# Optimization experiments

Measured on AMD Instinct MI355X. Metric: run time of the kernel, lower is better.

The kernel has to match this reference:

```python
import jax, jax.numpy as jnp
import numpy as np

N = 50000      # number of atoms/nodes
D = 32         # atom_dim == units (pad_length = 0)
E = 300000     # number of bonds/edges
BD = 16        # bond_dim
STEPS = 4      # message passing steps


def setup_inputs() -> dict:
    key = jax.random.key(0)
    ks = jax.random.split(key, 8)
    atom_features = jax.random.normal(ks[0], (N, D), dtype=jnp.float32)
    bond_features = jax.random.uniform(ks[1], (E, BD), dtype=jnp.float32)
    pair_indices = jax.random.randint(ks[2], (E, 2), 0, N, dtype=jnp.int32)
    # EdgeNetwork kernel: xavier_uniform on [bond_dim, atom_dim*atom_dim]
    s = float(np.sqrt(6.0 / (BD + D * D)))
    kernel = jax.random.uniform(ks[3], (BD, D * D), dtype=jnp.float32, minval=-s, maxval=s)
    bias = jnp.zeros((D * D,), dtype=jnp.float32)
    # torch.nn.GRUCell init: U(-1/sqrt(H), 1/sqrt(H)), H = D (pad_length = 0)
    stdv = float(1.0 / np.sqrt(D))
    W_ih = jax.random.uniform(ks[4], (3 * D, D), dtype=jnp.float32, minval=-stdv, maxval=stdv)
    W_hh = jax.random.uniform(ks[5], (3 * D, D), dtype=jnp.float32, minval=-stdv, maxval=stdv)
    b_ih = jax.random.uniform(ks[6], (3 * D,), dtype=jnp.float32, minval=-stdv, maxval=stdv)
    b_hh = jax.random.uniform(ks[7], (3 * D,), dtype=jnp.float32, minval=-stdv, maxval=stdv)
    return {
        "atom_features": atom_features,
        "bond_features": bond_features,
        "pair_indices": pair_indices,
        "kernel": kernel,
        "bias": bias,
        "W_ih": W_ih,
        "W_hh": W_hh,
        "b_ih": b_ih,
        "b_hh": b_hh,
    }


def _gru_cell(x, h, W_ih, W_hh, b_ih, b_hh):
    # torch.nn.GRUCell math, gates stacked as (r, z, n)
    gi = x @ W_ih.T + b_ih  # [N, 3D]
    gh = h @ W_hh.T + b_hh  # [N, 3D]
    i_r, i_z, i_n = jnp.split(gi, 3, axis=-1)
    h_r, h_z, h_n = jnp.split(gh, 3, axis=-1)
    r = jax.nn.sigmoid(i_r + h_r)
    z = jax.nn.sigmoid(i_z + h_z)
    n = jnp.tanh(i_n + r * h_n)
    return (1.0 - z) * n + z * h


def reference(atom_features, bond_features, pair_indices, kernel, bias, W_ih, W_hh, b_ih, b_hh):
    # pad_length = units - atom_dim = 0, so no padding needed.
    W = kernel.reshape(BD, D, D)   # per-bond-feature DxD transforms
    Bm = bias.reshape(D, D)        # bias as DxD matrix applied to neighbor feats
    dst = pair_indices[:, 0]       # aggregation (index_add) target
    src = pair_indices[:, 1]       # gathered neighbor

    h = atom_features
    for _ in range(STEPS):
        nbr = h[src]  # [E, D] gather
        # transformed[e, i] = sum_j (bond[e] @ kernel + bias)[i, j] * nbr[e, j]
        msg = jnp.einsum('eb,bij,ej->ei', bond_features, W, nbr) + nbr @ Bm.T
        agg = jax.ops.segment_sum(msg, dst, num_segments=N)  # scatter-add
        h = _gru_cell(agg, h, W_ih, W_hh, b_ih, b_hh)
    return h
```

## Files before the change

kernel.cpp:

```cpp
#include <hip/hip_runtime.h>
#include <math.h>

#define N_ATOMS 50000
#define D 32
#define E_EDGES 300000
#define BD 16
#define SW 544
#define SCAN_BLOCKS ((N_ATOMS + 255) / 256)
#define GRU_TILE 8
#define GRU_NT (N_ATOMS / GRU_TILE)

#define NB 32
#define FBLOCKS ((N_ATOMS + NB - 1) / NB)

__device__ __forceinline__ float sigmoidf_(float x) {
    return 1.0f / (1.0f + __expf(-x));
}


__global__ void k_build_wt(const float* __restrict__ kern,
                           const float* __restrict__ bias,
                           float* __restrict__ WTj) {
    int idx = blockIdx.x * 256 + threadIdx.x;
    if (idx >= 32 * SW) return;
    int j = idx / SW;
    int r = idx - j * SW;
    int b = r >> 5, i = r & 31;
    WTj[idx] = (b < BD) ? kern[b * 1024 + i * 32 + j] : bias[i * 32 + j];
}

__global__ void k_hist(const int* __restrict__ pair, int* __restrict__ deg) {
    int e = blockIdx.x * 256 + threadIdx.x;
    if (e < E_EDGES) atomicAdd(&deg[pair[2 * e + 1]], 1);
}

__global__ void k_scan1(const int* __restrict__ deg, int* __restrict__ offs,
                        int* __restrict__ bsums) {
    __shared__ int sm[256];
    int t = threadIdx.x, gid = blockIdx.x * 256 + t;
    int v = (gid < N_ATOMS) ? deg[gid] : 0;
    sm[t] = v;
    __syncthreads();
    for (int off = 1; off < 256; off <<= 1) {
        int x = (t >= off) ? sm[t - off] : 0;
        __syncthreads();
        sm[t] += x;
        __syncthreads();
    }
    if (gid < N_ATOMS) offs[gid] = sm[t] - v;
    if (t == 255) bsums[blockIdx.x] = sm[255];
}

__global__ void k_scan2(const int* __restrict__ bsums, int* __restrict__ boffs, int nb) {
    __shared__ int sm[256];
    int t = threadIdx.x;
    int v = (t < nb) ? bsums[t] : 0;
    sm[t] = v;
    __syncthreads();
    for (int off = 1; off < 256; off <<= 1) {
        int x = (t >= off) ? sm[t - off] : 0;
        __syncthreads();
        sm[t] += x;
        __syncthreads();
    }
    if (t < nb) boffs[t] = sm[t] - v;
}

__global__ void k_scan3(int* __restrict__ offs, const int* __restrict__ boffs) {
    int gid = blockIdx.x * 256 + threadIdx.x;
    if (gid < N_ATOMS) offs[gid] += boffs[blockIdx.x];
}

__global__ void k_scatter_perm(const int* __restrict__ pair, const int* __restrict__ offs,
                               int* __restrict__ cursor, const float* __restrict__ bond,
                               float* __restrict__ bond_perm, int* __restrict__ dst_perm) {
    int e = blockIdx.x * 256 + threadIdx.x;
    if (e >= E_EDGES) return;
    int d = pair[2 * e], s = pair[2 * e + 1];
    int pos = offs[s] + atomicAdd(&cursor[s], 1);
    dst_perm[pos] = d;
    const float4* src4 = (const float4*)(bond + (size_t)e * BD);
    float4* dst4 = (float4*)(bond_perm + (size_t)pos * BD);
    dst4[0] = src4[0];
    dst4[1] = src4[1];
    dst4[2] = src4[2];
    dst4[3] = src4[3];
}

#define EDGE_FMA(M, B0, B1, B2, B3, YN) do {            \
    M = fmaf(B0.x, YN[0],  M); M = fmaf(B0.y, YN[1],  M); \
    M = fmaf(B0.z, YN[2],  M); M = fmaf(B0.w, YN[3],  M); \
    M = fmaf(B1.x, YN[4],  M); M = fmaf(B1.y, YN[5],  M); \
    M = fmaf(B1.z, YN[6],  M); M = fmaf(B1.w, YN[7],  M); \
    M = fmaf(B2.x, YN[8],  M); M = fmaf(B2.y, YN[9],  M); \
    M = fmaf(B2.z, YN[10], M); M = fmaf(B2.w, YN[11], M); \
    M = fmaf(B3.x, YN[12], M); M = fmaf(B3.y, YN[13], M); \
    M = fmaf(B3.z, YN[14], M); M = fmaf(B3.w, YN[15], M); \
} while (0)

__global__ __launch_bounds__(256, 2)
void k_fused(const float* __restrict__ h_in, float* __restrict__ agg,
             const float* __restrict__ bond_perm, const int* __restrict__ dst_perm,
             const float* __restrict__ WTj,
             const int* __restrict__ offs, const int* __restrict__ deg) {
    __shared__ float h_lds[NB][33];

    const int t = threadIdx.x;
    const int bbase = blockIdx.x * NB;
    const int i = t & 31;
    const int grp = t >> 5;
    const int hn0 = grp * 4;

#pragma unroll
    for (int k = 0; k < 4; ++k) {
        const int idx = t + 256 * k;
        const int n = idx >> 5, j = idx & 31;
        const int node = bbase + n;
        h_lds[n][j] = (node < N_ATOMS) ? h_in[(size_t)node * D + j] : 0.f;
    }

    int stv[4], env[4];
#pragma unroll
    for (int n = 0; n < 4; ++n) {
        const int node = bbase + hn0 + n;
        const bool ok = (node < N_ATOMS);
        const int o = ok ? offs[node] : 0;
        stv[n] = o;
        env[n] = o + (ok ? deg[node] : 0);
    }
    __syncthreads();

    float y[4][17];
#pragma unroll
    for (int n = 0; n < 4; ++n)
#pragma unroll
        for (int b = 0; b < 17; ++b) y[n][b] = 0.f;

    for (int j = 0; j < 32; ++j) {
        float wv[17];
#pragma unroll
        for (int b = 0; b < 17; ++b)
            wv[b] = WTj[j * SW + b * 32 + i];
#pragma unroll
        for (int n = 0; n < 4; ++n) {
            const float hv = h_lds[hn0 + n][j];
#pragma unroll
            for (int b = 0; b < 17; ++b)
                y[n][b] = fmaf(wv[b], hv, y[n][b]);
        }
    }

#pragma unroll
    for (int n = 0; n < 4; ++n) {
        int p = stv[n];
        const int e = env[n];
        for (; p + 2 <= e; p += 2) {
            const float4* bp0 = (const float4*)(bond_perm + (size_t)p * BD);
            const float4* bp1 = (const float4*)(bond_perm + (size_t)(p + 1) * BD);
            const int d0 = dst_perm[p];
            const int d1 = dst_perm[p + 1];
            const float4 a0 = bp0[0], a1 = bp0[1], a2 = bp0[2], a3 = bp0[3];
            const float4 c0 = bp1[0], c1 = bp1[1], c2 = bp1[2], c3 = bp1[3];
            float m0 = y[n][16];
            float m1 = y[n][16];
            EDGE_FMA(m0, a0, a1, a2, a3, y[n]);
            EDGE_FMA(m1, c0, c1, c2, c3, y[n]);
            atomicAdd(&agg[(size_t)d0 * D + i], m0);
            atomicAdd(&agg[(size_t)d1 * D + i], m1);
        }
        if (p < e) {
            const float4* bp0 = (const float4*)(bond_perm + (size_t)p * BD);
            const int d0 = dst_perm[p];
            const float4 a0 = bp0[0], a1 = bp0[1], a2 = bp0[2], a3 = bp0[3];
            float m0 = y[n][16];
            EDGE_FMA(m0, a0, a1, a2, a3, y[n]);
            atomicAdd(&agg[(size_t)d0 * D + i], m0);
        }
    }
}

__global__ __launch_bounds__(256, 2)
void k_gru(float* __restrict__ agg_g, const float* __restrict__ h_in,
           float* __restrict__ h_out,
           const float* __restrict__ Wih, const float* __restrict__ Whh,
           const float* __restrict__ bih, const float* __restrict__ bhh) {
    __shared__ float Wih_s[96][33];
    __shared__ float Whh_s[96][33];
    __shared__ float bih_s[96], bhh_s[96];
    __shared__ float x_lds[GRU_TILE][32];
    __shared__ float h_lds[GRU_TILE][32];

    const int t = threadIdx.x;

    for (int idx = t; idx < 96 * 32; idx += 256) {
        const int o = idx >> 5, jj = idx & 31;
        Wih_s[o][jj] = Wih[idx];
        Whh_s[o][jj] = Whh[idx];
    }
    if (t < 96) { bih_s[t] = bih[t]; bhh_s[t] = bhh[t]; }

    const int r = t >> 5;
    const int i = t & 31;
    const int stride = gridDim.x;

    int tile = blockIdx.x;
    float xr = 0.f, hr = 0.f;
    if (tile < GRU_NT) {
        xr = agg_g[tile * 256 + t];
        hr = h_in[tile * 256 + t];
    }
    for (; tile < GRU_NT; tile += stride) {
        ((float*)x_lds)[t] = xr;
        ((float*)h_lds)[t] = hr;
        agg_g[tile * 256 + t] = 0.f;
        __syncthreads();
        const int nxt = tile + stride;
        if (nxt < GRU_NT) {
            xr = agg_g[nxt * 256 + t];
            hr = h_in[nxt * 256 + t];
        }
        float gri = bih_s[i],      grh = bhh_s[i];
        float gzi = bih_s[32 + i], gzh = bhh_s[32 + i];
        float gni = bih_s[64 + i], gnh = bhh_s[64 + i];
#pragma unroll 8
        for (int jj = 0; jj < 32; ++jj) {
            const float xv = x_lds[r][jj];
            const float hv = h_lds[r][jj];
            gri = fmaf(Wih_s[i][jj],      xv, gri);
            gzi = fmaf(Wih_s[32 + i][jj], xv, gzi);
            gni = fmaf(Wih_s[64 + i][jj], xv, gni);
            grh = fmaf(Whh_s[i][jj],      hv, grh);
            gzh = fmaf(Whh_s[32 + i][jj], hv, gzh);
            gnh = fmaf(Whh_s[64 + i][jj], hv, gnh);
        }
        const float rg = sigmoidf_(gri + grh);
        const float zg = sigmoidf_(gzi + gzh);
        float xn = gni + rg * gnh;
        xn = fminf(fmaxf(xn, -15.f), 15.f);
        const float e2 = __expf(2.f * xn);
        const float ng = (e2 - 1.f) / (e2 + 1.f);
        h_out[tile * 256 + t] = (1.f - zg) * ng + zg * h_lds[r][i];
        __syncthreads();
    }
}

extern "C" void kernel_launch(void* const* d_in, const int* in_sizes, int n_in,
                              void* d_out, int out_size, void* d_ws, size_t ws_size,
                              hipStream_t stream) {
    const float* atom = (const float*)d_in[0];
    const float* bond = (const float*)d_in[1];
    const int*   pair = (const int*)d_in[2];
    const float* kern = (const float*)d_in[3];
    const float* bias = (const float*)d_in[4];
    const float* Wih  = (const float*)d_in[5];
    const float* Whh  = (const float*)d_in[6];
    const float* bih  = (const float*)d_in[7];
    const float* bhh  = (const float*)d_in[8];
    float* out = (float*)d_out;

    char* w = (char*)d_ws;
    auto alloc = [&](size_t bytes) {
        char* p = w;
        w += (bytes + 255) & ~size_t(255);
        return p;
    };
    float* hA        = (float*)alloc((size_t)N_ATOMS * D * 4);
    float* aggG      = (float*)alloc((size_t)N_ATOMS * D * 4);
    float* WTj       = (float*)alloc((size_t)32 * SW * 4);
    int*   deg       = (int*)alloc((size_t)N_ATOMS * 4);
    int*   offs      = (int*)alloc((size_t)N_ATOMS * 4);
    int*   cursor    = (int*)alloc((size_t)N_ATOMS * 4);
    int*   bsums     = (int*)alloc(256 * 4);
    int*   boffs     = (int*)alloc(256 * 4);
    int*   dst_perm  = (int*)alloc((size_t)E_EDGES * 4);
    float* bond_perm = (float*)alloc((size_t)E_EDGES * BD * 4);

    hipMemsetAsync(deg, 0, (size_t)N_ATOMS * 4, stream);
    hipMemsetAsync(cursor, 0, (size_t)N_ATOMS * 4, stream);
    hipMemsetAsync(aggG, 0, (size_t)N_ATOMS * D * 4, stream);

    k_build_wt<<<(32 * SW + 255) / 256, 256, 0, stream>>>(kern, bias, WTj);
    k_hist<<<(E_EDGES + 255) / 256, 256, 0, stream>>>(pair, deg);
    k_scan1<<<SCAN_BLOCKS, 256, 0, stream>>>(deg, offs, bsums);
    k_scan2<<<1, 256, 0, stream>>>(bsums, boffs, SCAN_BLOCKS);
    k_scan3<<<SCAN_BLOCKS, 256, 0, stream>>>(offs, boffs);
    k_scatter_perm<<<(E_EDGES + 255) / 256, 256, 0, stream>>>(pair, offs, cursor,
                                                              bond, bond_perm, dst_perm);

    const float* hsrc = atom;
    float* hdst[4] = { hA, out, hA, out };
    for (int s = 0; s < 4; ++s) {
        k_fused<<<FBLOCKS, 256, 0, stream>>>(hsrc, aggG, bond_perm, dst_perm,
                                             WTj, offs, deg);
        k_gru<<<2048, 256, 0, stream>>>(aggG, hsrc, hdst[s], Wih, Whh, bih, bhh);
        hsrc = hdst[s];
    }
}
```

Before: 496.8 us.

## Replace atomic scatter-add with dst-sorted message buffer and segmented reduction

Builds a second CSR grouped by destination node and computes, for each source-sorted edge, its slot in destination order. The message kernel then writes each edge message to that slot with a plain store instead of an atomicAdd. The GRU kernel reduces each node's contiguous message range before the gate math, which also removes the aggregate-buffer memset and the zeroing pass. In exchange it adds a 38 MB message buffer that is written and read every step, plus extra setup kernels for the second histogram, scan and position pass.

```diff
diff --git a/kernel.cpp b/kernel.cpp
--- a/kernel.cpp
+++ b/kernel.cpp
@@ -29,9 +29,9 @@
     WTj[idx] = (b < BD) ? kern[b * 1024 + i * 32 + j] : bias[i * 32 + j];
 }
 
-__global__ void k_hist(const int* __restrict__ pair, int* __restrict__ deg) {
+__global__ void k_hist(const int* __restrict__ pair, int* __restrict__ deg, int col) {
     int e = blockIdx.x * 256 + threadIdx.x;
-    if (e < E_EDGES) atomicAdd(&deg[pair[2 * e + 1]], 1);
+    if (e < E_EDGES) atomicAdd(&deg[pair[2 * e + col]], 1);
 }
 
 __global__ void k_scan1(const int* __restrict__ deg, int* __restrict__ offs,
@@ -73,18 +73,26 @@
 
 __global__ void k_scatter_perm(const int* __restrict__ pair, const int* __restrict__ offs,
                                int* __restrict__ cursor, const float* __restrict__ bond,
-                               float* __restrict__ bond_perm, int* __restrict__ dst_perm) {
+                               float* __restrict__ bond_perm, int* __restrict__ dstid) {
     int e = blockIdx.x * 256 + threadIdx.x;
     if (e >= E_EDGES) return;
     int d = pair[2 * e], s = pair[2 * e + 1];
     int pos = offs[s] + atomicAdd(&cursor[s], 1);
-    dst_perm[pos] = d;
+    dstid[pos] = d;
     const float4* src4 = (const float4*)(bond + (size_t)e * BD);
     float4* dst4 = (float4*)(bond_perm + (size_t)pos * BD);
     dst4[0] = src4[0];
     dst4[1] = src4[1];
     dst4[2] = src4[2];
     dst4[3] = src4[3];
+}
+
+__global__ void k_dstpos(const int* __restrict__ dstid, const int* __restrict__ offs2,
+                         int* __restrict__ cursor2, int* __restrict__ wpos) {
+    int p = blockIdx.x * 256 + threadIdx.x;
+    if (p >= E_EDGES) return;
+    int d = dstid[p];
+    wpos[p] = offs2[d] + atomicAdd(&cursor2[d], 1);
 }
 
 #define EDGE_FMA(M, B0, B1, B2, B3, YN) do {            \
@@ -99,10 +107,10 @@
 } while (0)
 
 __global__ __launch_bounds__(256, 2)
-void k_fused(const float* __restrict__ h_in, float* __restrict__ agg,
-             const float* __restrict__ bond_perm, const int* __restrict__ dst_perm,
-             const float* __restrict__ WTj,
-             const int* __restrict__ offs, const int* __restrict__ deg) {
+void k_msg(const float* __restrict__ h_in, float* __restrict__ msg_d,
+           const float* __restrict__ bond_perm, const int* __restrict__ wpos,
+           const float* __restrict__ WTj,
+           const int* __restrict__ offs, const int* __restrict__ deg) {
     __shared__ float h_lds[NB][33];
 
     const int t = threadIdx.x;
@@ -157,33 +165,34 @@
         for (; p + 2 <= e; p += 2) {
             const float4* bp0 = (const float4*)(bond_perm + (size_t)p * BD);
             const float4* bp1 = (const float4*)(bond_perm + (size_t)(p + 1) * BD);
-            const int d0 = dst_perm[p];
-            const int d1 = dst_perm[p + 1];
+            const int w0 = wpos[p];
+            const int w1 = wpos[p + 1];
             const float4 a0 = bp0[0], a1 = bp0[1], a2 = bp0[2], a3 = bp0[3];
             const float4 c0 = bp1[0], c1 = bp1[1], c2 = bp1[2], c3 = bp1[3];
             float m0 = y[n][16];
             float m1 = y[n][16];
             EDGE_FMA(m0, a0, a1, a2, a3, y[n]);
             EDGE_FMA(m1, c0, c1, c2, c3, y[n]);
-            atomicAdd(&agg[(size_t)d0 * D + i], m0);
-            atomicAdd(&agg[(size_t)d1 * D + i], m1);
+            msg_d[(size_t)w0 * D + i] = m0;
+            msg_d[(size_t)w1 * D + i] = m1;
         }
         if (p < e) {
             const float4* bp0 = (const float4*)(bond_perm + (size_t)p * BD);
-            const int d0 = dst_perm[p];
+            const int w0 = wpos[p];
             const float4 a0 = bp0[0], a1 = bp0[1], a2 = bp0[2], a3 = bp0[3];
             float m0 = y[n][16];
             EDGE_FMA(m0, a0, a1, a2, a3, y[n]);
-            atomicAdd(&agg[(size_t)d0 * D + i], m0);
+            msg_d[(size_t)w0 * D + i] = m0;
         }
     }
 }
 
 __global__ __launch_bounds__(256, 2)
-void k_gru(float* __restrict__ agg_g, const float* __restrict__ h_in,
-           float* __restrict__ h_out,
-           const float* __restrict__ Wih, const float* __restrict__ Whh,
-           const float* __restrict__ bih, const float* __restrict__ bhh) {
+void k_aggru(const float* __restrict__ msg_d,
+             const int* __restrict__ offs2, const int* __restrict__ deg2,
+             const float* __restrict__ h_in, float* __restrict__ h_out,
+             const float* __restrict__ Wih, const float* __restrict__ Whh,
+             const float* __restrict__ bih, const float* __restrict__ bhh) {
     __shared__ float Wih_s[96][33];
     __shared__ float Whh_s[96][33];
     __shared__ float bih_s[96], bhh_s[96];
@@ -203,22 +212,24 @@
     const int i = t & 31;
     const int stride = gridDim.x;
 
-    int tile = blockIdx.x;
-    float xr = 0.f, hr = 0.f;
-    if (tile < GRU_NT) {
-        xr = agg_g[tile * 256 + t];
-        hr = h_in[tile * 256 + t];
-    }
-    for (; tile < GRU_NT; tile += stride) {
-        ((float*)x_lds)[t] = xr;
-        ((float*)h_lds)[t] = hr;
-        agg_g[tile * 256 + t] = 0.f;
-        __syncthreads();
-        const int nxt = tile + stride;
-        if (nxt < GRU_NT) {
-            xr = agg_g[nxt * 256 + t];
-            hr = h_in[nxt * 256 + t];
-        }
+    for (int tile = blockIdx.x; tile < GRU_NT; tile += stride) {
+        const int node = tile * GRU_TILE + r;
+        const int st = offs2[node];
+        const int en = st + deg2[node];
+        float acc = 0.f;
+        int p = st;
+        for (; p + 4 <= en; p += 4) {
+            const float a0 = msg_d[(size_t)(p + 0) * D + i];
+            const float a1 = msg_d[(size_t)(p + 1) * D + i];
+            const float a2 = msg_d[(size_t)(p + 2) * D + i];
+            const float a3 = msg_d[(size_t)(p + 3) * D + i];
+            acc += (a0 + a1) + (a2 + a3);
+        }
+        for (; p < en; ++p) acc += msg_d[(size_t)p * D + i];
+        x_lds[r][i] = acc;
+        ((float*)h_lds)[t] = h_in[tile * 256 + t];
+        __syncthreads();
+
         float gri = bih_s[i],      grh = bhh_s[i];
         float gzi = bih_s[32 + i], gzh = bhh_s[32 + i];
         float gni = bih_s[64 + i], gnh = bhh_s[64 + i];
@@ -265,34 +276,45 @@
         return p;
     };
     float* hA        = (float*)alloc((size_t)N_ATOMS * D * 4);
-    float* aggG      = (float*)alloc((size_t)N_ATOMS * D * 4);
     float* WTj       = (float*)alloc((size_t)32 * SW * 4);
     int*   deg       = (int*)alloc((size_t)N_ATOMS * 4);
     int*   offs      = (int*)alloc((size_t)N_ATOMS * 4);
+    int*   deg2      = (int*)alloc((size_t)N_ATOMS * 4);
+    int*   offs2     = (int*)alloc((size_t)N_ATOMS * 4);
     int*   cursor    = (int*)alloc((size_t)N_ATOMS * 4);
+    int*   cursor2   = (int*)alloc((size_t)N_ATOMS * 4);
     int*   bsums     = (int*)alloc(256 * 4);
     int*   boffs     = (int*)alloc(256 * 4);
-    int*   dst_perm  = (int*)alloc((size_t)E_EDGES * 4);
+    int*   dstid     = (int*)alloc((size_t)E_EDGES * 4);
+    int*   wpos      = (int*)alloc((size_t)E_EDGES * 4);
     float* bond_perm = (float*)alloc((size_t)E_EDGES * BD * 4);
+    float* msg_d     = (float*)alloc((size_t)E_EDGES * D * 4);
 
     hipMemsetAsync(deg, 0, (size_t)N_ATOMS * 4, stream);
+    hipMemsetAsync(deg2, 0, (size_t)N_ATOMS * 4, stream);
     hipMemsetAsync(cursor, 0, (size_t)N_ATOMS * 4, stream);
-    hipMemsetAsync(aggG, 0, (size_t)N_ATOMS * D * 4, stream);
+    hipMemsetAsync(cursor2, 0, (size_t)N_ATOMS * 4, stream);
 
     k_build_wt<<<(32 * SW + 255) / 256, 256, 0, stream>>>(kern, bias, WTj);
-    k_hist<<<(E_EDGES + 255) / 256, 256, 0, stream>>>(pair, deg);
+    k_hist<<<(E_EDGES + 255) / 256, 256, 0, stream>>>(pair, deg, 1);
     k_scan1<<<SCAN_BLOCKS, 256, 0, stream>>>(deg, offs, bsums);
     k_scan2<<<1, 256, 0, stream>>>(bsums, boffs, SCAN_BLOCKS);
     k_scan3<<<SCAN_BLOCKS, 256, 0, stream>>>(offs, boffs);
+    k_hist<<<(E_EDGES + 255) / 256, 256, 0, stream>>>(pair, deg2, 0);
+    k_scan1<<<SCAN_BLOCKS, 256, 0, stream>>>(deg2, offs2, bsums);
+    k_scan2<<<1, 256, 0, stream>>>(bsums, boffs, SCAN_BLOCKS);
+    k_scan3<<<SCAN_BLOCKS, 256, 0, stream>>>(offs2, boffs);
     k_scatter_perm<<<(E_EDGES + 255) / 256, 256, 0, stream>>>(pair, offs, cursor,
-                                                              bond, bond_perm, dst_perm);
+                                                              bond, bond_perm, dstid);
+    k_dstpos<<<(E_EDGES + 255) / 256, 256, 0, stream>>>(dstid, offs2, cursor2, wpos);
 
     const float* hsrc = atom;
     float* hdst[4] = { hA, out, hA, out };
     for (int s = 0; s < 4; ++s) {
-        k_fused<<<FBLOCKS, 256, 0, stream>>>(hsrc, aggG, bond_perm, dst_perm,
-                                             WTj, offs, deg);
-        k_gru<<<2048, 256, 0, stream>>>(aggG, hsrc, hdst[s], Wih, Whh, bih, bhh);
+        k_msg<<<FBLOCKS, 256, 0, stream>>>(hsrc, msg_d, bond_perm, wpos,
+                                           WTj, offs, deg);
+        k_aggru<<<2048, 256, 0, stream>>>(msg_d, offs2, deg2, hsrc, hdst[s],
+                                          Wih, Whh, bih, bhh);
         hsrc = hdst[s];
     }
 }
```

Measured after the change: 564.2 us. +13.6%, slower.

## Fuse message-passing steps into a persistent cooperative kernel with grid syncs

Applied to the files above, without the earlier changes.

Replaces the eight per-step launches (edge kernel plus GRU kernel per step) with one cooperative persistent kernel. It loops over tiles grid-stride and uses grid-wide syncs between the edge phase and the GRU phase. GRU weights are loaded into shared memory once for all steps, and the deg/cursor buffers are merged into one padded allocation so a single memset clears both and the scan bounds checks can go. The trade-off is a grid capped at 1024 blocks, tied to occupancy, which may leave the edge phase with less parallelism than the original 1563-block launch, and the GRU register prefetch is gone. A fallback keeps the separate-launch path if the cooperative launch fails.

```diff
diff --git a/kernel.cpp b/kernel.cpp
--- a/kernel.cpp
+++ b/kernel.cpp
@@ -1,17 +1,22 @@
 #include <hip/hip_runtime.h>
+#include <hip/hip_cooperative_groups.h>
 #include <math.h>
+
+namespace cg = cooperative_groups;
 
 #define N_ATOMS 50000
 #define D 32
 #define E_EDGES 300000
 #define BD 16
 #define SW 544
-#define SCAN_BLOCKS ((N_ATOMS + 255) / 256)
+#define PADN 50176
+#define SCAN_BLOCKS 196
 #define GRU_TILE 8
 #define GRU_NT (N_ATOMS / GRU_TILE)
 
 #define NB 32
-#define FBLOCKS ((N_ATOMS + NB - 1) / NB)
+#define FT ((N_ATOMS + NB - 1) / NB)
+#define FBLOCKS FT
 
 __device__ __forceinline__ float sigmoidf_(float x) {
     return 1.0f / (1.0f + __expf(-x));
@@ -38,7 +43,7 @@
                         int* __restrict__ bsums) {
     __shared__ int sm[256];
     int t = threadIdx.x, gid = blockIdx.x * 256 + t;
-    int v = (gid < N_ATOMS) ? deg[gid] : 0;
+    int v = deg[gid];
     sm[t] = v;
     __syncthreads();
     for (int off = 1; off < 256; off <<= 1) {
@@ -47,7 +52,7 @@
         sm[t] += x;
         __syncthreads();
     }
-    if (gid < N_ATOMS) offs[gid] = sm[t] - v;
+    offs[gid] = sm[t] - v;
     if (t == 255) bsums[blockIdx.x] = sm[255];
 }
 
@@ -68,17 +73,17 @@
 
 __global__ void k_scan3(int* __restrict__ offs, const int* __restrict__ boffs) {
     int gid = blockIdx.x * 256 + threadIdx.x;
-    if (gid < N_ATOMS) offs[gid] += boffs[blockIdx.x];
+    offs[gid] += boffs[blockIdx.x];
 }
 
 __global__ void k_scatter_perm(const int* __restrict__ pair, const int* __restrict__ offs,
                                int* __restrict__ cursor, const float* __restrict__ bond,
-                               float* __restrict__ bond_perm, int* __restrict__ dst_perm) {
+                               float* __restrict__ bond_perm, int* __restrict__ dstid) {
     int e = blockIdx.x * 256 + threadIdx.x;
     if (e >= E_EDGES) return;
     int d = pair[2 * e], s = pair[2 * e + 1];
     int pos = offs[s] + atomicAdd(&cursor[s], 1);
-    dst_perm[pos] = d;
+    dstid[pos] = d;
     const float4* src4 = (const float4*)(bond + (size_t)e * BD);
     float4* dst4 = (float4*)(bond_perm + (size_t)pos * BD);
     dst4[0] = src4[0];
@@ -98,27 +103,22 @@
     M = fmaf(B3.z, YN[14], M); M = fmaf(B3.w, YN[15], M); \
 } while (0)
 
-__global__ __launch_bounds__(256, 2)
-void k_fused(const float* __restrict__ h_in, float* __restrict__ agg,
-             const float* __restrict__ bond_perm, const int* __restrict__ dst_perm,
-             const float* __restrict__ WTj,
-             const int* __restrict__ offs, const int* __restrict__ deg) {
-    __shared__ float h_lds[NB][33];
-
-    const int t = threadIdx.x;
-    const int bbase = blockIdx.x * NB;
-    const int i = t & 31;
-    const int grp = t >> 5;
-    const int hn0 = grp * 4;
-
+
+__device__ __forceinline__ void fused_tile_body(
+        int tile, int t, int i, int hn0,
+        const float* __restrict__ hs, float* __restrict__ agg,
+        const float* __restrict__ bond_perm, const int* __restrict__ dstid,
+        const float* __restrict__ WTj,
+        const int* __restrict__ offs, const int* __restrict__ deg,
+        float (*h_lds)[33]) {
+    const int bbase = tile * NB;
 #pragma unroll
     for (int k = 0; k < 4; ++k) {
         const int idx = t + 256 * k;
         const int n = idx >> 5, j = idx & 31;
         const int node = bbase + n;
-        h_lds[n][j] = (node < N_ATOMS) ? h_in[(size_t)node * D + j] : 0.f;
-    }
-
+        h_lds[n][j] = (node < N_ATOMS) ? hs[(size_t)node * D + j] : 0.f;
+    }
     int stv[4], env[4];
 #pragma unroll
     for (int n = 0; n < 4; ++n) {
@@ -157,8 +157,8 @@
         for (; p + 2 <= e; p += 2) {
             const float4* bp0 = (const float4*)(bond_perm + (size_t)p * BD);
             const float4* bp1 = (const float4*)(bond_perm + (size_t)(p + 1) * BD);
-            const int d0 = dst_perm[p];
-            const int d1 = dst_perm[p + 1];
+            const int d0 = dstid[p];
+            const int d1 = dstid[p + 1];
             const float4 a0 = bp0[0], a1 = bp0[1], a2 = bp0[2], a3 = bp0[3];
             const float4 c0 = bp1[0], c1 = bp1[1], c2 = bp1[2], c3 = bp1[3];
             float m0 = y[n][16];
@@ -170,13 +170,110 @@
         }
         if (p < e) {
             const float4* bp0 = (const float4*)(bond_perm + (size_t)p * BD);
-            const int d0 = dst_perm[p];
+            const int d0 = dstid[p];
             const float4 a0 = bp0[0], a1 = bp0[1], a2 = bp0[2], a3 = bp0[3];
             float m0 = y[n][16];
             EDGE_FMA(m0, a0, a1, a2, a3, y[n]);
             atomicAdd(&agg[(size_t)d0 * D + i], m0);
         }
     }
+}
+
+__device__ __forceinline__ void gru_tile_body(
+        int tile, int t, int r, int i,
+        float* __restrict__ agg, const float* __restrict__ hs,
+        float* __restrict__ hd,
+        const float (*Wih_s)[33], const float (*Whh_s)[33],
+        const float* bih_s, const float* bhh_s,
+        float (*xg)[32], float (*hg)[32]) {
+    ((float*)xg)[t] = agg[tile * 256 + t];
+    ((float*)hg)[t] = hs[tile * 256 + t];
+    agg[tile * 256 + t] = 0.f;
+    __syncthreads();
+
+    float gri = bih_s[i],      grh = bhh_s[i];
+    float gzi = bih_s[32 + i], gzh = bhh_s[32 + i];
+    float gni = bih_s[64 + i], gnh = bhh_s[64 + i];
+#pragma unroll 8
+    for (int jj = 0; jj < 32; ++jj) {
+        const float xv = xg[r][jj];
+        const float hv = hg[r][jj];
+        gri = fmaf(Wih_s[i][jj],      xv, gri);
+        gzi = fmaf(Wih_s[32 + i][jj], xv, gzi);
+        gni = fmaf(Wih_s[64 + i][jj], xv, gni);
+        grh = fmaf(Whh_s[i][jj],      hv, grh);
+        gzh = fmaf(Whh_s[32 + i][jj], hv, gzh);
+        gnh = fmaf(Whh_s[64 + i][jj], hv, gnh);
+    }
+    const float rg = sigmoidf_(gri + grh);
+    const float zg = sigmoidf_(gzi + gzh);
+    float xn = gni + rg * gnh;
+    xn = fminf(fmaxf(xn, -15.f), 15.f);
+    const float e2 = __expf(2.f * xn);
+    const float ng = (e2 - 1.f) / (e2 + 1.f);
+    hd[tile * 256 + t] = (1.f - zg) * ng + zg * hg[r][i];
+}
+
+__global__ __launch_bounds__(256, 2)
+void k_mega(const float* __restrict__ atom, float* __restrict__ hA,
+            float* __restrict__ outp, float* __restrict__ agg,
+            const float* __restrict__ bond_perm, const int* __restrict__ dstid,
+            const float* __restrict__ WTj,
+            const int* __restrict__ offs, const int* __restrict__ deg,
+            const float* __restrict__ Wih, const float* __restrict__ Whh,
+            const float* __restrict__ bih, const float* __restrict__ bhh) {
+    cg::grid_group gg = cg::this_grid();
+
+    __shared__ float Wih_s[96][33];
+    __shared__ float Whh_s[96][33];
+    __shared__ float bih_s[96], bhh_s[96];
+    __shared__ float h_lds[NB][33];
+    __shared__ float xg[GRU_TILE][32];
+    __shared__ float hg[GRU_TILE][32];
+
+    const int t = threadIdx.x;
+    const int i = t & 31;
+    const int grp = t >> 5;
+    const int hn0 = grp * 4;
+    const int r = t >> 5;
+    const int G = (int)gridDim.x;
+
+    for (int idx = t; idx < 96 * 32; idx += 256) {
+        const int o = idx >> 5, jj = idx & 31;
+        Wih_s[o][jj] = Wih[idx];
+        Whh_s[o][jj] = Whh[idx];
+    }
+    if (t < 96) { bih_s[t] = bih[t]; bhh_s[t] = bhh[t]; }
+
+    for (int s = 0; s < 4; ++s) {
+        const float* hs = (s == 0) ? atom : ((s & 1) ? hA : outp);
+        float* hd = (s & 1) ? outp : hA;
+
+        for (int tile = blockIdx.x; tile < FT; tile += G) {
+            __syncthreads();
+            fused_tile_body(tile, t, i, hn0, hs, agg, bond_perm, dstid,
+                            WTj, offs, deg, h_lds);
+        }
+        gg.sync();
+
+        for (int tile = blockIdx.x; tile < GRU_NT; tile += G) {
+            __syncthreads();
+            gru_tile_body(tile, t, r, i, agg, hs, hd,
+                          Wih_s, Whh_s, bih_s, bhh_s, xg, hg);
+        }
+        gg.sync();
+    }
+}
+
+__global__ __launch_bounds__(256, 2)
+void k_fused(const float* __restrict__ h_in, float* __restrict__ agg,
+             const float* __restrict__ bond_perm, const int* __restrict__ dstid,
+             const float* __restrict__ WTj,
+             const int* __restrict__ offs, const int* __restrict__ deg) {
+    __shared__ float h_lds[NB][33];
+    const int t = threadIdx.x;
+    fused_tile_body(blockIdx.x, t, t & 31, (t >> 5) * 4, h_in, agg,
+                    bond_perm, dstid, WTj, offs, deg, h_lds);
 }
 
 __global__ __launch_bounds__(256, 2)
@@ -187,60 +284,22 @@
     __shared__ float Wih_s[96][33];
     __shared__ float Whh_s[96][33];
     __shared__ float bih_s[96], bhh_s[96];
-    __shared__ float x_lds[GRU_TILE][32];
-    __shared__ float h_lds[GRU_TILE][32];
+    __shared__ float xg[GRU_TILE][32];
+    __shared__ float hg[GRU_TILE][32];
 
     const int t = threadIdx.x;
-
     for (int idx = t; idx < 96 * 32; idx += 256) {
         const int o = idx >> 5, jj = idx & 31;
         Wih_s[o][jj] = Wih[idx];
         Whh_s[o][jj] = Whh[idx];
     }
     if (t < 96) { bih_s[t] = bih[t]; bhh_s[t] = bhh[t]; }
-
-    const int r = t >> 5;
-    const int i = t & 31;
-    const int stride = gridDim.x;
-
-    int tile = blockIdx.x;
-    float xr = 0.f, hr = 0.f;
-    if (tile < GRU_NT) {
-        xr = agg_g[tile * 256 + t];
-        hr = h_in[tile * 256 + t];
-    }
-    for (; tile < GRU_NT; tile += stride) {
-        ((float*)x_lds)[t] = xr;
-        ((float*)h_lds)[t] = hr;
-        agg_g[tile * 256 + t] = 0.f;
-        __syncthreads();
-        const int nxt = tile + stride;
-        if (nxt < GRU_NT) {
-            xr = agg_g[nxt * 256 + t];
-            hr = h_in[nxt * 256 + t];
-        }
-        float gri = bih_s[i],      grh = bhh_s[i];
-        float gzi = bih_s[32 + i], gzh = bhh_s[32 + i];
-        float gni = bih_s[64 + i], gnh = bhh_s[64 + i];
-#pragma unroll 8
-        for (int jj = 0; jj < 32; ++jj) {
-            const float xv = x_lds[r][jj];
-            const float hv = h_lds[r][jj];
-            gri = fmaf(Wih_s[i][jj],      xv, gri);
-            gzi = fmaf(Wih_s[32 + i][jj], xv, gzi);
-            gni = fmaf(Wih_s[64 + i][jj], xv, gni);
-            grh = fmaf(Whh_s[i][jj],      hv, grh);
-            gzh = fmaf(Whh_s[32 + i][jj], hv, gzh);
-            gnh = fmaf(Whh_s[64 + i][jj], hv, gnh);
-        }
-        const float rg = sigmoidf_(gri + grh);
-        const float zg = sigmoidf_(gzi + gzh);
-        float xn = gni + rg * gnh;
-        xn = fminf(fmaxf(xn, -15.f), 15.f);
-        const float e2 = __expf(2.f * xn);
-        const float ng = (e2 - 1.f) / (e2 + 1.f);
-        h_out[tile * 256 + t] = (1.f - zg) * ng + zg * h_lds[r][i];
-        __syncthreads();
+    const int r = t >> 5, i = t & 31;
+
+    for (int tile = blockIdx.x; tile < GRU_NT; tile += gridDim.x) {
+        __syncthreads();
+        gru_tile_body(tile, t, r, i, agg_g, h_in, h_out,
+                      Wih_s, Whh_s, bih_s, bhh_s, xg, hg);
     }
 }
 
@@ -267,16 +326,16 @@
     float* hA        = (float*)alloc((size_t)N_ATOMS * D * 4);
     float* aggG      = (float*)alloc((size_t)N_ATOMS * D * 4);
     float* WTj       = (float*)alloc((size_t)32 * SW * 4);
-    int*   deg       = (int*)alloc((size_t)N_ATOMS * 4);
-    int*   offs      = (int*)alloc((size_t)N_ATOMS * 4);
-    int*   cursor    = (int*)alloc((size_t)N_ATOMS * 4);
+    int*   degcur    = (int*)alloc((size_t)2 * PADN * 4);
+    int*   offs      = (int*)alloc((size_t)PADN * 4);
     int*   bsums     = (int*)alloc(256 * 4);
     int*   boffs     = (int*)alloc(256 * 4);
-    int*   dst_perm  = (int*)alloc((size_t)E_EDGES * 4);
+    int*   dstid     = (int*)alloc((size_t)E_EDGES * 4);
     float* bond_perm = (float*)alloc((size_t)E_EDGES * BD * 4);
-
-    hipMemsetAsync(deg, 0, (size_t)N_ATOMS * 4, stream);
-    hipMemsetAsync(cursor, 0, (size_t)N_ATOMS * 4, stream);
+    int* deg    = degcur;
+    int* cursor = degcur + PADN;
+
+    hipMemsetAsync(degcur, 0, (size_t)2 * PADN * 4, stream);
     hipMemsetAsync(aggG, 0, (size_t)N_ATOMS * D * 4, stream);
 
     k_build_wt<<<(32 * SW + 255) / 256, 256, 0, stream>>>(kern, bias, WTj);
@@ -285,14 +344,35 @@
     k_scan2<<<1, 256, 0, stream>>>(bsums, boffs, SCAN_BLOCKS);
     k_scan3<<<SCAN_BLOCKS, 256, 0, stream>>>(offs, boffs);
     k_scatter_perm<<<(E_EDGES + 255) / 256, 256, 0, stream>>>(pair, offs, cursor,
-                                                              bond, bond_perm, dst_perm);
-
-    const float* hsrc = atom;
-    float* hdst[4] = { hA, out, hA, out };
-    for (int s = 0; s < 4; ++s) {
-        k_fused<<<FBLOCKS, 256, 0, stream>>>(hsrc, aggG, bond_perm, dst_perm,
-                                             WTj, offs, deg);
-        k_gru<<<2048, 256, 0, stream>>>(aggG, hsrc, hdst[s], Wih, Whh, bih, bhh);
-        hsrc = hdst[s];
-    }
-}
+                                                              bond, bond_perm, dstid);
+
+    int dev = 0;
+    (void)hipGetDevice(&dev);
+    int numCU = 0;
+    (void)hipDeviceGetAttribute(&numCU, hipDeviceAttributeMultiprocessorCount, dev);
+    int maxBpCU = 0;
+    (void)hipOccupancyMaxActiveBlocksPerMultiprocessor(&maxBpCU, (const void*)k_mega, 256, 0);
+    long maxGrid = (long)numCU * (long)maxBpCU;
+    int grid = (int)((maxGrid > 0) ? (maxGrid < 1024 ? maxGrid : 1024) : 0);
+
+    hipError_t cerr = hipErrorUnknown;
+    if (grid >= 64) {
+        void* args[] = { (void*)&atom, (void*)&hA, (void*)&out, (void*)&aggG,
+                         (void*)&bond_perm, (void*)&dstid, (void*)&WTj,
+                         (void*)&offs, (void*)&deg,
+                         (void*)&Wih, (void*)&Whh, (void*)&bih, (void*)&bhh };
+        cerr = hipLaunchCooperativeKernel((void*)k_mega, dim3(grid), dim3(256),
+                                          args, 0, stream);
+    }
+    if (cerr != hipSuccess) {
+        (void)hipGetLastError();
+        const float* hsrc = atom;
+        float* hdst[4] = { hA, out, hA, out };
+        for (int s = 0; s < 4; ++s) {
+            k_fused<<<FBLOCKS, 256, 0, stream>>>(hsrc, aggG, bond_perm, dstid,
+                                                 WTj, offs, deg);
+            k_gru<<<768, 256, 0, stream>>>(aggG, hsrc, hdst[s], Wih, Whh, bih, bhh);
+            hsrc = hdst[s];
+        }
+    }
+}
```

Result: slower. 1.010 ms (+103.4%).
